# Kernel optimization log

Hardware: AMD Instinct MI355X
Metric: run time of the kernel (lower is better)

The kernel has to match this reference:

```python
import jax, jax.numpy as jnp
import numpy as np

C = 512
NUM_GROUPS = 32
EPS = 1e-6


def group_norm(x, gamma, beta):
    # x: [B, C, H, W]
    B, Cc, H, W = x.shape
    xg = x.reshape(B, NUM_GROUPS, Cc // NUM_GROUPS, H, W)
    mean = xg.mean(axis=(2, 3, 4), keepdims=True)
    var = xg.var(axis=(2, 3, 4), keepdims=True)
    xn = (xg - mean) / jnp.sqrt(var + EPS)
    xn = xn.reshape(B, Cc, H, W)
    return xn * gamma[None, :, None, None] + beta[None, :, None, None]


def conv1x1(x, w, b):
    # w: [out_c, in_c], x: [B, C, H, W]
    return jnp.einsum('oc,bchw->bohw', w, x) + b[None, :, None, None]


def setup_inputs() -> dict:
    key = jax.random.key(0)
    ks = jax.random.split(key, 6)
    B, H, W = 2, 64, 64
    x = jax.random.normal(ks[0], (B, C, H, W), dtype=jnp.float32)
    s = 1.0 / np.sqrt(C)
    wq = jax.random.normal(ks[1], (C, C), dtype=jnp.float32) * s
    wk = jax.random.normal(ks[2], (C, C), dtype=jnp.float32) * s
    wv = jax.random.normal(ks[3], (C, C), dtype=jnp.float32) * s
    wo = jax.random.normal(ks[4], (C, C), dtype=jnp.float32) * s
    bq = jnp.zeros((C,), jnp.float32)
    bk = jnp.zeros((C,), jnp.float32)
    bv = jnp.zeros((C,), jnp.float32)
    bo = jnp.zeros((C,), jnp.float32)
    gamma = jnp.ones((C,), jnp.float32)
    beta = jnp.zeros((C,), jnp.float32)
    return {"x": x, "gamma": gamma, "beta": beta, "wq": wq, "bq": bq,
            "wk": wk, "bk": bk, "wv": wv, "bv": bv, "wo": wo, "bo": bo}


def reference(x, gamma, beta, wq, bq, wk, bk, wv, bv, wo, bo):
    B, Cc, H, W = x.shape
    h = group_norm(x, gamma, beta)
    q = conv1x1(h, wq, bq).reshape(B, Cc, H * W)  # [B, C, N]
    k = conv1x1(h, wk, bk).reshape(B, Cc, H * W)
    v = conv1x1(h, wv, bv).reshape(B, Cc, H * W)
    scale = Cc ** (-0.5)
    # scores a[b,i,j] = sum_c q[b,c,i] * k[b,c,j]
    a = jnp.einsum('bci,bcj->bij', q, k) * scale
    a = jax.nn.softmax(a, axis=2)
    # out[b,c,i] = sum_j v[b,c,j] * a[b,i,j]  (matches bmm(v, a^T))
    o = jnp.einsum('bcj,bij->bci', v, a).reshape(B, Cc, H, W)
    o = conv1x1(o, wo, bo)
    return x + o
```

## Files before the change

kernel.cpp:

```cpp
#include <hip/hip_runtime.h>
#include <stdint.h>

#define NPIX 4096
#define CDIM 512

typedef _Float16 hv8 __attribute__((ext_vector_type(8)));
typedef float f32x4 __attribute__((ext_vector_type(4)));

__device__ __forceinline__ void lds_direct16(const _Float16* g, _Float16* l) {
    __builtin_amdgcn_global_load_lds(
        (const __attribute__((address_space(1))) void*)g,
        (__attribute__((address_space(3))) void*)l, 16, 0, 0);
}

__global__ void pstats_kernel(const float* __restrict__ x,
                              float* __restrict__ partS, float* __restrict__ partQ,
                              const float* __restrict__ wq, const float* __restrict__ wk,
                              const float* __restrict__ wv, const float* __restrict__ wo,
                              _Float16* __restrict__ d0, _Float16* __restrict__ d1,
                              _Float16* __restrict__ d2, _Float16* __restrict__ d3,
                              const float* __restrict__ bq, const float* __restrict__ bk,
                              float* __restrict__ bqk) {
    int pb = blockIdx.x;
    int tid = threadIdx.x;

#pragma unroll
    for (int h = 0; h < 2; ++h) {
        int ii = pb * 512 + h * 256 + tid;
        d0[ii] = (_Float16)wq[ii];
        d1[ii] = (_Float16)wk[ii];
        d2[ii] = (_Float16)wv[ii];
        d3[ii] = (_Float16)wo[ii];
        if (ii < 512) bqk[ii] = bq[ii];
        else if (ii < 1024) bqk[ii] = bk[ii - 512];
    }

    int gi = pb >> 3;
    int sl = pb & 7;
    const float4* base = (const float4*)x + (long)gi * 16384 + sl * 2048;
    float s = 0.f, sq = 0.f;
    for (int it = 0; it < 8; ++it) {
        float4 f = base[it * 256 + tid];
        s  += f.x + f.y + f.z + f.w;
        sq += f.x * f.x + f.y * f.y + f.z * f.z + f.w * f.w;
    }
    __shared__ float rs[256], rq[256];
    rs[tid] = s; rq[tid] = sq;
    __syncthreads();
    for (int st = 128; st > 0; st >>= 1) {
        if (tid < st) { rs[tid] += rs[tid + st]; rq[tid] += rq[tid + st]; }
        __syncthreads();
    }
    if (tid == 0) { partS[pb] = rs[0]; partQ[pb] = rq[0]; }
}

__global__ void normT_kernel(const float* __restrict__ x,
                             const float* __restrict__ partS, const float* __restrict__ partQ,
                             const float* __restrict__ gamma, const float* __restrict__ beta,
                             _Float16* __restrict__ hT) {
    int b = blockIdx.z, c0 = blockIdx.x * 32, n0 = blockIdx.y * 32;
    int tid = threadIdx.x;
    __shared__ float t[32][33];
    int cl = tid >> 5;
    int nl = tid & 31;
    for (int r = 0; r < 4; ++r)
        t[r * 8 + cl][nl] = x[(long)b * CDIM * NPIX + (long)(c0 + r * 8 + cl) * NPIX + n0 + nl];
    __syncthreads();
    int c = c0 + nl;
    int gg = b * 32 + (c >> 4);
    float s = 0.f, q = 0.f;
#pragma unroll
    for (int k2 = 0; k2 < 8; ++k2) { s += partS[gg * 8 + k2]; q += partQ[gg * 8 + k2]; }
    float m    = s * (1.0f / 65536.0f);
    float rstd = rsqrtf(q * (1.0f / 65536.0f) - m * m + 1e-6f);
    float gm = gamma[c], bt = beta[c];
    for (int r = 0; r < 4; ++r) {
        int nr = r * 8 + cl;
        float val = (t[nl][nr] - m) * rstd * gm + bt;
        hT[(long)b * NPIX * CDIM + (long)(n0 + nr) * CDIM + c] = (_Float16)val;
    }
}

template<int EPI>
__launch_bounds__(256, 2)
__global__ void gemm_bt_kernel(const _Float16* __restrict__ A, const _Float16* __restrict__ BT,
                               void* __restrict__ D, const float* __restrict__ bias,
                               int M, int N, int K,
                               long aBatch, long bBatch, long dBatch) {
    const int b = blockIdx.z;
    A  += (long)b * aBatch;
    BT += (long)b * bBatch;
    const int m0 = blockIdx.y * 128;
    const int n0 = blockIdx.x * 128;
    const int tid = threadIdx.x;
    const int l = tid & 63;
    const int w = tid >> 6;
    const int wm = (w >> 1) * 64;
    const int wn = (w & 1) * 64;
    const int lr = l & 15;
    const int lk = l >> 4;
    __shared__ __align__(16) _Float16 As[128 * 32];
    __shared__ __align__(16) _Float16 Bs[128 * 32];
    f32x4 acc[4][4] = {};
    const int nK = K >> 5;
    for (int kt = 0; kt < nK; ++kt) {
        const int kb = kt * 32;
#pragma unroll
        for (int c = 0; c < 2; ++c) {
            int chunk = c * 256 + tid;
            int row = chunk >> 2;
            int k8 = (chunk & 3) * 8;
            _Float16* ldsA = As + (size_t)(c * 256 + (tid & ~63)) * 8;
            _Float16* ldsB = Bs + (size_t)(c * 256 + (tid & ~63)) * 8;
            lds_direct16(A  + (long)(m0 + row) * K + kb + k8, ldsA);
            lds_direct16(BT + (long)(n0 + row) * K + kb + k8, ldsB);
        }
        __syncthreads();
        hv8 af[4], bfr[4];
#pragma unroll
        for (int mi = 0; mi < 4; ++mi)
            af[mi] = *(const hv8*)(As + (size_t)(wm + mi * 16 + lr) * 32 + lk * 8);
#pragma unroll
        for (int ni = 0; ni < 4; ++ni)
            bfr[ni] = *(const hv8*)(Bs + (size_t)(wn + ni * 16 + lr) * 32 + lk * 8);
#pragma unroll
        for (int mi = 0; mi < 4; ++mi)
#pragma unroll
            for (int ni = 0; ni < 4; ++ni)
                acc[mi][ni] = __builtin_amdgcn_mfma_f32_16x16x32_f16(af[mi], bfr[ni], acc[mi][ni], 0, 0, 0);
        __syncthreads();
    }
#pragma unroll
    for (int mi = 0; mi < 4; ++mi)
#pragma unroll
        for (int ni = 0; ni < 4; ++ni)
#pragma unroll
            for (int r = 0; r < 4; ++r) {
                int row = m0 + wm + mi * 16 + lk * 4 + r;
                int col = n0 + wn + ni * 16 + lr;
                float val = acc[mi][ni][r];
                if (EPI == 1) {
                    ((_Float16*)D)[(long)b * dBatch + (long)row * N + col] = (_Float16)(val + bias[row]);
                } else {
                    long qoff = (long)(col >> 9) * (2L * NPIX * CDIM);
                    ((_Float16*)D)[qoff + (long)b * dBatch + (long)row * CDIM + (col & 511)] =
                        (_Float16)(val + bias[col]);
                }
            }
}

__launch_bounds__(256, 2)
__global__ void gemm_final_kernel(const _Float16* __restrict__ A,
                                  const _Float16* __restrict__ p0,
                                  const _Float16* __restrict__ p1,
                                  const float* __restrict__ lbuf,
                                  float* __restrict__ D, const float* __restrict__ bias,
                                  const float* __restrict__ resid) {
    const int b = blockIdx.z;
    const int m0 = blockIdx.y * 128;
    const int n0 = blockIdx.x * 128;
    const int tid = threadIdx.x;
    const int l = tid & 63;
    const int w = tid >> 6;
    const int wm = (w >> 1) * 64;
    const int wn = (w & 1) * 64;
    const int lr = l & 15;
    const int lk = l >> 4;
    __shared__ __align__(16) _Float16 As[128 * 32];
    __shared__ __align__(16) _Float16 Bs[128 * 32];
    __shared__ float wA[128], wB[128];

    if (tid < 128) {
        int rowg = b * NPIX + n0 + tid;
        float l0 = lbuf[rowg], l1 = lbuf[8192 + rowg];
        float inv = 1.0f / (l0 + l1);
        wA[tid] = l0 * inv;
        wB[tid] = l1 * inv;
    }
    __syncthreads();

    const _Float16* pb0 = p0 + (long)b * NPIX * CDIM;
    const _Float16* pb1 = p1 + (long)b * NPIX * CDIM;

    f32x4 acc[4][4] = {};
    for (int kt = 0; kt < 16; ++kt) {
        const int kb = kt * 32;
#pragma unroll
        for (int c = 0; c < 2; ++c) {
            int chunk = c * 256 + tid;
            int row = chunk >> 2;
            int k8 = (chunk & 3) * 8;
            _Float16* ldsA = As + (size_t)(c * 256 + (tid & ~63)) * 8;
            lds_direct16(A + (long)(m0 + row) * CDIM + kb + k8, ldsA);
            long goff = (long)(n0 + row) * CDIM + kb + k8;
            hv8 va = *(const hv8*)(pb0 + goff);
            hv8 vb = *(const hv8*)(pb1 + goff);
            float w0 = wA[row], w1 = wB[row];
            hv8 vo;
#pragma unroll
            for (int i = 0; i < 8; ++i)
                vo[i] = (_Float16)((float)va[i] * w0 + (float)vb[i] * w1);
            *(hv8*)(Bs + (size_t)chunk * 8) = vo;
        }
        __syncthreads();
        hv8 af[4], bfr[4];
#pragma unroll
        for (int mi = 0; mi < 4; ++mi)
            af[mi] = *(const hv8*)(As + (size_t)(wm + mi * 16 + lr) * 32 + lk * 8);
#pragma unroll
        for (int ni = 0; ni < 4; ++ni)
            bfr[ni] = *(const hv8*)(Bs + (size_t)(wn + ni * 16 + lr) * 32 + lk * 8);
#pragma unroll
        for (int mi = 0; mi < 4; ++mi)
#pragma unroll
            for (int ni = 0; ni < 4; ++ni)
                acc[mi][ni] = __builtin_amdgcn_mfma_f32_16x16x32_f16(af[mi], bfr[ni], acc[mi][ni], 0, 0, 0);
        __syncthreads();
    }
#pragma unroll
    for (int mi = 0; mi < 4; ++mi)
#pragma unroll
        for (int ni = 0; ni < 4; ++ni)
#pragma unroll
            for (int r = 0; r < 4; ++r) {
                int row = m0 + wm + mi * 16 + lk * 4 + r;
                int col = n0 + wn + ni * 16 + lr;
                long idx = (long)row * NPIX + col;
                D[(long)b * NPIX * CDIM + idx] =
                    acc[mi][ni][r] + bias[row] + resid[(long)b * NPIX * CDIM + idx];
            }
}

__launch_bounds__(512, 2)
__global__ void attn_kernel(const _Float16* __restrict__ qT, const _Float16* __restrict__ kT,
                            const _Float16* __restrict__ v,
                            _Float16* __restrict__ p0, _Float16* __restrict__ p1,
                            float* __restrict__ lbuf) {
    __shared__ __align__(16) _Float16 Ks[2][32 * 512];
    __shared__ __align__(16) char ps[2][64 * 80];
    __shared__ float red[8][64];
    __shared__ float redt[64];

    const int g = blockIdx.x;
    const int xcd = g & 7;
    const int comb = xcd >> 1;
    const int itile = ((g >> 3) << 1) | (xcd & 1);
    const int batch = comb >> 1;
    const int jhalf = comb & 1;
    const int i0 = itile * 64;
    const int jbase = jhalf * 2048;

    const int tid = threadIdx.x;
    const int l = tid & 63, w = tid >> 6;
    const int lr = l & 15, lk = l >> 4;
    const int iq = w >> 1, jq = w & 1;

    const _Float16* qb = qT + (long)batch * NPIX * CDIM;
    const _Float16* kb = kT + (long)batch * NPIX * CDIM;
    const _Float16* vb = v  + (long)batch * CDIM * NPIX;

    hv8 af[16];
    {
        const _Float16* qr = qb + (long)(i0 + iq * 16 + lr) * CDIM + lk * 8;
#pragma unroll
        for (int kk = 0; kk < 16; ++kk)
            af[kk] = *(const hv8*)(qr + kk * 32);
    }

    f32x4 oacc[4][4] = {};
    float lsum[4] = {};
    hv8 vf[4];

    const _Float16* vptr = vb + (long)(w * 64 + lr) * NPIX + jbase + lk * 8;
    const float scale = 0.044194173824159216f;

#define STAGE(BUF, JT)                                                               \
    {                                                                                \
        const long j0s = (long)jbase + (JT) * 32;                                    \
        _Float16* kd = Ks[BUF];                                                      \
        _Pragma("unroll")                                                            \
        for (int q = 0; q < 4; ++q) {                                                \
            int row = q * 8 + w;                                                     \
            int cc = l ^ (row & 7);                                                  \
            lds_direct16(kb + (j0s + row) * CDIM + cc * 8, kd + row * 512);          \
        }                                                                            \
    }

#define VLOAD(JT)                                                                    \
    {                                                                                \
        _Pragma("unroll")                                                            \
        for (int ni = 0; ni < 4; ++ni)                                               \
            vf[ni] = *(const hv8*)(vptr + (long)ni * (16 * NPIX) + (JT) * 32);       \
    }

#define QKEXP(CUR)                                                                   \
    {                                                                                \
        const char* kbase = (const char*)Ks[CUR];                                    \
        f32x4 sa = {}, sb = {};                                                      \
        const int jj = jq * 16 + lr;                                                 \
        const uint32_t sw = (uint32_t)((jj & 7) << 4);                               \
        _Pragma("unroll")                                                            \
        for (int kk = 0; kk < 8; ++kk) {                                             \
            hv8 b0 = *(const hv8*)(kbase + (((uint32_t)(jj * 1024 + (2 * kk) * 64 + lk * 16)) ^ sw));     \
            sa = __builtin_amdgcn_mfma_f32_16x16x32_f16(af[2 * kk], b0, sa, 0, 0, 0);                     \
            hv8 b1 = *(const hv8*)(kbase + (((uint32_t)(jj * 1024 + (2 * kk + 1) * 64 + lk * 16)) ^ sw)); \
            sb = __builtin_amdgcn_mfma_f32_16x16x32_f16(af[2 * kk + 1], b1, sb, 0, 0, 0);                 \
        }                                                                            \
        sa += sb;                                                                    \
        _Pragma("unroll")                                                            \
        for (int r = 0; r < 4; ++r) {                                                \
            float p = __expf(sa[r] * scale);                                         \
            lsum[r] += p;                                                            \
            int i = iq * 16 + lk * 4 + r;                                            \
            int j2 = jq * 16 + lr;                                                   \
            *(_Float16*)(ps[CUR] + i * 80 + j2 * 2) = (_Float16)p;                   \
        }                                                                            \
    }

#define PVSTEP(PRV)                                                                  \
    {                                                                                \
        _Pragma("unroll")                                                            \
        for (int mi = 0; mi < 4; ++mi) {                                             \
            int i2 = mi * 16 + lr;                                                   \
            hv8 pa = *(const hv8*)(ps[PRV] + i2 * 80 + lk * 16);                     \
            _Pragma("unroll")                                                        \
            for (int ni = 0; ni < 4; ++ni)                                           \
                oacc[mi][ni] = __builtin_amdgcn_mfma_f32_16x16x32_f16(pa, vf[ni], oacc[mi][ni], 0, 0, 0); \
        }                                                                            \
    }

#define ENDBAR(N)                                                                    \
    __builtin_amdgcn_sched_barrier(0);                                               \
    asm volatile("s_waitcnt vmcnt(" #N ") lgkmcnt(0)" ::: "memory");                 \
    __builtin_amdgcn_s_barrier();                                                    \
    __builtin_amdgcn_sched_barrier(0);

#define STEP(JT, CUR)                                                                \
    {                                                                                \
        if ((JT) < 63) STAGE((CUR) ^ 1, (JT) + 1)                                    \
        __builtin_amdgcn_sched_barrier(0);                                           \
        __builtin_amdgcn_s_setprio(1);                                               \
        QKEXP(CUR)                                                                   \
        PVSTEP((CUR) ^ 1)                                                            \
        __builtin_amdgcn_s_setprio(0);                                               \
        __builtin_amdgcn_sched_barrier(0);                                           \
        VLOAD(JT)                                                                    \
        ENDBAR(4)                                                                    \
    }

    STAGE(0, 0)
    __builtin_amdgcn_sched_barrier(0);
    asm volatile("s_waitcnt vmcnt(0)" ::: "memory");
    __builtin_amdgcn_s_barrier();
    __builtin_amdgcn_sched_barrier(0);

    STAGE(1, 1)
    __builtin_amdgcn_s_setprio(1);
    QKEXP(0)
    __builtin_amdgcn_s_setprio(0);
    VLOAD(0)
    ENDBAR(4)

    for (int jt = 1; jt < 63; jt += 2) {
        STEP(jt,     1)
        STEP(jt + 1, 0)
    }
    STEP(63, 1)

    asm volatile("s_waitcnt vmcnt(0)" ::: "memory");
    __builtin_amdgcn_sched_barrier(0);
    PVSTEP(1)

#pragma unroll
    for (int m = 1; m <= 8; m <<= 1)
#pragma unroll
        for (int r = 0; r < 4; ++r)
            lsum[r] += __shfl_xor(lsum[r], m, 64);
    if (lr == 0)
#pragma unroll
        for (int r = 0; r < 4; ++r)
            red[w][iq * 16 + lk * 4 + r] = lsum[r];
    __syncthreads();
    if (tid < 64) {
        int iq2 = tid >> 4;
        float lv = red[iq2 * 2][tid] + red[iq2 * 2 + 1][tid];
        redt[tid] = 1.0f / lv;
        lbuf[jhalf * 8192 + batch * NPIX + i0 + tid] = lv;
    }
    __syncthreads();

    _Float16* dsth = (jhalf ? p1 : p0) + (long)batch * NPIX * CDIM;
#pragma unroll
    for (int mi = 0; mi < 4; ++mi)
#pragma unroll
        for (int r = 0; r < 4; ++r) {
            int row = mi * 16 + lk * 4 + r;
            float rv = redt[row];
#pragma unroll
            for (int ni = 0; ni < 4; ++ni) {
                int c = w * 64 + ni * 16 + lr;
                dsth[(long)(i0 + row) * CDIM + c] = (_Float16)(oacc[mi][ni][r] * rv);
            }
        }
#undef STEP
#undef ENDBAR
#undef PVSTEP
#undef QKEXP
#undef VLOAD
#undef STAGE
}

extern "C" void kernel_launch(void* const* d_in, const int* in_sizes, int n_in,
                              void* d_out, int out_size, void* d_ws, size_t ws_size,
                              hipStream_t stream) {
    const float* x     = (const float*)d_in[0];
    const float* gamma = (const float*)d_in[1];
    const float* beta  = (const float*)d_in[2];
    const float* wq    = (const float*)d_in[3];
    const float* bq    = (const float*)d_in[4];
    const float* wk    = (const float*)d_in[5];
    const float* bk    = (const float*)d_in[6];
    const float* wv    = (const float*)d_in[7];
    const float* bv    = (const float*)d_in[8];
    const float* wo    = (const float*)d_in[9];
    const float* bo    = (const float*)d_in[10];
    float* out = (float*)d_out;

    char* ws = (char*)d_ws;
    float* partS = (float*)ws;
    float* partQ = partS + 512;
    float* bqk   = partQ + 512;
    _Float16* wqb = (_Float16*)(ws + 8192);
    _Float16* wkb = wqb + 262144;
    _Float16* wvb = wkb + 262144;
    _Float16* wob = wvb + 262144;
    _Float16* hT  = wob + 262144;
    const long TSZ = (long)2 * NPIX * CDIM;
    _Float16* qT = hT + TSZ;
    _Float16* kT = qT + TSZ;
    _Float16* vv = kT + TSZ;
    _Float16* oT = vv + TSZ;
    float* lbuf = (float*)(oT + TSZ);

    pstats_kernel<<<dim3(512), dim3(256), 0, stream>>>(
        x, partS, partQ, wq, wk, wv, wo, wqb, wkb, wvb, wob, bq, bk, bqk);
    normT_kernel<<<dim3(16, 128, 2), dim3(256), 0, stream>>>(x, partS, partQ, gamma, beta, hT);

    const long NC = (long)NPIX * CDIM;
    gemm_bt_kernel<3><<<dim3(8, 32, 2), dim3(256), 0, stream>>>(
        hT, wqb, (void*)qT, bqk, NPIX, 1024, CDIM, NC, 0L, NC);
    gemm_bt_kernel<1><<<dim3(32, 4, 2), dim3(256), 0, stream>>>(
        wvb, hT, (void*)vv, bv, CDIM, NPIX, CDIM, 0L, NC, NC);

    attn_kernel<<<dim3(256), dim3(512), 0, stream>>>(qT, kT, vv, oT, hT, lbuf);

    gemm_final_kernel<<<dim3(32, 4, 2), dim3(256), 0, stream>>>(
        wob, oT, hT, lbuf, out, bo, x);
}
```

Baseline: 177.8 us.

## Split attention key range into four quarters for more blocks

```diff
diff --git a/kernel.cpp b/kernel.cpp
--- a/kernel.cpp
+++ b/kernel.cpp
@@ -153,6 +153,8 @@
 __global__ void gemm_final_kernel(const _Float16* __restrict__ A,
                                   const _Float16* __restrict__ p0,
                                   const _Float16* __restrict__ p1,
+                                  const _Float16* __restrict__ p2,
+                                  const _Float16* __restrict__ p3,
                                   const float* __restrict__ lbuf,
                                   float* __restrict__ D, const float* __restrict__ bias,
                                   const float* __restrict__ resid) {
@@ -168,19 +170,22 @@
     const int lk = l >> 4;
     __shared__ __align__(16) _Float16 As[128 * 32];
     __shared__ __align__(16) _Float16 Bs[128 * 32];
-    __shared__ float wA[128], wB[128];
+    __shared__ float wt[4][128];
 
     if (tid < 128) {
         int rowg = b * NPIX + n0 + tid;
         float l0 = lbuf[rowg], l1 = lbuf[8192 + rowg];
-        float inv = 1.0f / (l0 + l1);
-        wA[tid] = l0 * inv;
-        wB[tid] = l1 * inv;
+        float l2 = lbuf[16384 + rowg], l3 = lbuf[24576 + rowg];
+        float inv = 1.0f / (l0 + l1 + l2 + l3);
+        wt[0][tid] = l0 * inv; wt[1][tid] = l1 * inv;
+        wt[2][tid] = l2 * inv; wt[3][tid] = l3 * inv;
     }
     __syncthreads();
 
     const _Float16* pb0 = p0 + (long)b * NPIX * CDIM;
     const _Float16* pb1 = p1 + (long)b * NPIX * CDIM;
+    const _Float16* pb2 = p2 + (long)b * NPIX * CDIM;
+    const _Float16* pb3 = p3 + (long)b * NPIX * CDIM;
 
     f32x4 acc[4][4] = {};
     for (int kt = 0; kt < 16; ++kt) {
@@ -195,11 +200,14 @@
             long goff = (long)(n0 + row) * CDIM + kb + k8;
             hv8 va = *(const hv8*)(pb0 + goff);
             hv8 vb = *(const hv8*)(pb1 + goff);
-            float w0 = wA[row], w1 = wB[row];
+            hv8 vc = *(const hv8*)(pb2 + goff);
+            hv8 vd = *(const hv8*)(pb3 + goff);
+            float w0 = wt[0][row], w1 = wt[1][row], w2 = wt[2][row], w3 = wt[3][row];
             hv8 vo;
 #pragma unroll
             for (int i = 0; i < 8; ++i)
-                vo[i] = (_Float16)((float)va[i] * w0 + (float)vb[i] * w1);
+                vo[i] = (_Float16)((float)va[i] * w0 + (float)vb[i] * w1
+                                 + (float)vc[i] * w2 + (float)vd[i] * w3);
             *(hv8*)(Bs + (size_t)chunk * 8) = vo;
         }
         __syncthreads();
@@ -235,6 +243,7 @@
 __global__ void attn_kernel(const _Float16* __restrict__ qT, const _Float16* __restrict__ kT,
                             const _Float16* __restrict__ v,
                             _Float16* __restrict__ p0, _Float16* __restrict__ p1,
+                            _Float16* __restrict__ p2, _Float16* __restrict__ p3,
                             float* __restrict__ lbuf) {
     __shared__ __align__(16) _Float16 Ks[2][32 * 512];
     __shared__ __align__(16) char ps[2][64 * 80];
@@ -243,12 +252,11 @@
 
     const int g = blockIdx.x;
     const int xcd = g & 7;
-    const int comb = xcd >> 1;
-    const int itile = ((g >> 3) << 1) | (xcd & 1);
-    const int batch = comb >> 1;
-    const int jhalf = comb & 1;
+    const int batch = xcd >> 2;
+    const int jq4 = xcd & 3;
+    const int itile = g >> 3;
     const int i0 = itile * 64;
-    const int jbase = jhalf * 2048;
+    const int jbase = jq4 * 1024;
 
     const int tid = threadIdx.x;
     const int l = tid & 63, w = tid >> 6;
@@ -337,7 +345,7 @@
 
 #define STEP(JT, CUR)                                                                \
     {                                                                                \
-        if ((JT) < 63) STAGE((CUR) ^ 1, (JT) + 1)                                    \
+        if ((JT) < 31) STAGE((CUR) ^ 1, (JT) + 1)                                    \
         __builtin_amdgcn_sched_barrier(0);                                           \
         __builtin_amdgcn_s_setprio(1);                                               \
         QKEXP(CUR)                                                                   \
@@ -361,11 +369,11 @@
     VLOAD(0)
     ENDBAR(4)
 
-    for (int jt = 1; jt < 63; jt += 2) {
+    for (int jt = 1; jt < 31; jt += 2) {
         STEP(jt,     1)
         STEP(jt + 1, 0)
     }
-    STEP(63, 1)
+    STEP(31, 1)
 
     asm volatile("s_waitcnt vmcnt(0)" ::: "memory");
     __builtin_amdgcn_sched_barrier(0);
@@ -385,11 +393,12 @@
         int iq2 = tid >> 4;
         float lv = red[iq2 * 2][tid] + red[iq2 * 2 + 1][tid];
         redt[tid] = 1.0f / lv;
-        lbuf[jhalf * 8192 + batch * NPIX + i0 + tid] = lv;
+        lbuf[jq4 * 8192 + batch * NPIX + i0 + tid] = lv;
     }
     __syncthreads();
 
-    _Float16* dsth = (jhalf ? p1 : p0) + (long)batch * NPIX * CDIM;
+    _Float16* dsth = (jq4 == 0 ? p0 : jq4 == 1 ? p1 : jq4 == 2 ? p2 : p3)
+                   + (long)batch * NPIX * CDIM;
 #pragma unroll
     for (int mi = 0; mi < 4; ++mi)
 #pragma unroll
@@ -441,6 +450,8 @@
     _Float16* vv = kT + TSZ;
     _Float16* oT = vv + TSZ;
     float* lbuf = (float*)(oT + TSZ);
+    _Float16* pq2 = (_Float16*)(lbuf + 32768);
+    _Float16* pq3 = pq2 + TSZ;
 
     pstats_kernel<<<dim3(512), dim3(256), 0, stream>>>(
         x, partS, partQ, wq, wk, wv, wo, wqb, wkb, wvb, wob, bq, bk, bqk);
@@ -452,8 +463,8 @@
     gemm_bt_kernel<1><<<dim3(32, 4, 2), dim3(256), 0, stream>>>(
         wvb, hT, (void*)vv, bv, CDIM, NPIX, CDIM, 0L, NC, NC);
 
-    attn_kernel<<<dim3(256), dim3(512), 0, stream>>>(qT, kT, vv, oT, hT, lbuf);
+    attn_kernel<<<dim3(512), dim3(512), 0, stream>>>(qT, kT, vv, oT, hT, pq2, pq3, lbuf);
 
     gemm_final_kernel<<<dim3(32, 4, 2), dim3(256), 0, stream>>>(
-        wob, oT, hT, lbuf, out, bo, x);
-}
+        wob, oT, hT, pq2, pq3, lbuf, out, bo, x);
+}
```

New measurement: 191.5 us. 1.08x slower.
